# Performance work log

Measured on AMD Instinct MI355X. Metric: run time of the kernel, lower is better.

The kernel has to match this reference:

```python
import jax, jax.numpy as jnp
import numpy as np

B, T, U, V = 8, 128, 64, 1024
BLANK = V - 1  # blank=-1 resolves to last class index


def setup_inputs() -> dict:
    key = jax.random.key(0)
    k1, k2, k3, k4 = jax.random.split(key, 4)
    logits = jax.random.normal(k1, (B, T, U + 1, V), dtype=jnp.float32)
    targets = jax.random.randint(k2, (B, U), 0, V - 1, dtype=jnp.int32)  # exclude blank
    logit_lengths = jax.random.randint(k3, (B,), T // 2, T + 1, dtype=jnp.int32)
    target_lengths = jax.random.randint(k4, (B,), U // 2, U + 1, dtype=jnp.int32)
    return {
        "logits": logits,
        "targets": targets,
        "logit_lengths": logit_lengths,
        "target_lengths": target_lengths,
    }


def _rnnt_neglogp(logits, targets, logit_lengths, target_lengths, blank):
    """RNNT forward-variable DP (Graves 2012). Returns per-sample -log p(y|x)."""
    Bn, Tn, U1, Vn = logits.shape
    Un = U1 - 1
    lp = jax.nn.log_softmax(logits, axis=-1)  # fused_log_softmax=True
    lp_blank = lp[..., blank]                                  # (B, T, U+1)
    idx = jnp.broadcast_to(targets[:, None, :, None], (Bn, Tn, Un, 1))
    lp_emit = jnp.take_along_axis(lp[:, :, :Un, :], idx, axis=-1)[..., 0]  # (B, T, U)

    # alpha[t, u]: log-prob of emitting first u labels using first t frames.
    # alpha[0, u] = sum_{v<u} emit(0, v)
    row0 = jnp.concatenate(
        [jnp.zeros((Bn, 1), lp.dtype), jnp.cumsum(lp_emit[:, 0, :], axis=-1)], axis=1
    )  # (B, U+1)

    def inner(a_prev, x):
        # a[u] = logaddexp(alpha[t-1,u] + blank(t-1,u),  a[u-1] + emit(t,u-1))
        b_u, e_u = x
        a_new = jnp.logaddexp(b_u, a_prev + e_u)
        return a_new, a_new

    def outer(prev_row, x):
        blank_prev, emit_t = x  # (B, U+1), (B, U)
        b_term = prev_row + blank_prev  # vertical (blank) transition term
        _, rest = jax.lax.scan(
            inner, b_term[:, 0], (b_term[:, 1:].T, emit_t.T)
        )  # rest: (U, B)
        new_row = jnp.concatenate([b_term[:, :1], rest.T], axis=1)  # (B, U+1)
        return new_row, new_row

    xs = (
        jnp.swapaxes(lp_blank[:, :-1, :], 0, 1),  # (T-1, B, U+1)
        jnp.swapaxes(lp_emit[:, 1:, :], 0, 1),    # (T-1, B, U)
    )
    _, rows = jax.lax.scan(outer, row0, xs)
    alpha = jnp.concatenate([row0[None], rows], axis=0)  # (T, B, U+1)

    bidx = jnp.arange(Bn)
    t_last = logit_lengths - 1
    u_last = target_lengths
    a_end = alpha[t_last, bidx, u_last]
    final_blank = lp_blank[bidx, t_last, u_last]
    return -(a_end + final_blank)


def reference(logits, targets, logit_lengths, target_lengths):
    return _rnnt_neglogp(logits, targets, logit_lengths, target_lengths, BLANK)
```

## Files before the change

### kernel.cpp

```cpp
#include <hip/hip_runtime.h>
#include <hip/hip_bf16.h>

#define BB 8
#define TT 128
#define UU 64
#define VV 1024
#define U1 65
#define NROWS (BB * TT * U1)
#define NDIAG (TT + UU)
#define DSZ (NDIAG * U1)
#define CD 48
#define CH_F4 ((CD * U1) / 2)

__device__ __forceinline__ float wave_max64(float v) {
#pragma unroll
    for (int off = 32; off; off >>= 1) v = fmaxf(v, __shfl_xor(v, off, 64));
    return v;
}
__device__ __forceinline__ float wave_sum64(float v) {
#pragma unroll
    for (int off = 32; off; off >>= 1) v += __shfl_xor(v, off, 64);
    return v;
}

__global__ __launch_bounds__(256) void rnnt_lse_kernel(
    const float* __restrict__ logits, const int* __restrict__ targets,
    float2* __restrict__ P) {
    const int wave = threadIdx.x >> 6;
    const int lane = threadIdx.x & 63;
    const int row  = blockIdx.x * 4 + wave;
    const float4* p4 = (const float4*)(logits + (size_t)row * VV);

    float4 x0 = p4[lane];
    float4 x1 = p4[lane + 64];
    float4 x2 = p4[lane + 128];
    float4 x3 = p4[lane + 192];

    float m = fmaxf(fmaxf(fmaxf(x0.x, x0.y), fmaxf(x0.z, x0.w)),
                    fmaxf(fmaxf(x1.x, x1.y), fmaxf(x1.z, x1.w)));
    m = fmaxf(m, fmaxf(fmaxf(fmaxf(x2.x, x2.y), fmaxf(x2.z, x2.w)),
                       fmaxf(fmaxf(x3.x, x3.y), fmaxf(x3.z, x3.w))));
    m = wave_max64(m);

    float s = __expf(x0.x - m) + __expf(x0.y - m) + __expf(x0.z - m) + __expf(x0.w - m)
            + __expf(x1.x - m) + __expf(x1.y - m) + __expf(x1.z - m) + __expf(x1.w - m)
            + __expf(x2.x - m) + __expf(x2.y - m) + __expf(x2.z - m) + __expf(x2.w - m)
            + __expf(x3.x - m) + __expf(x3.y - m) + __expf(x3.z - m) + __expf(x3.w - m);
    s = wave_sum64(s);
    const float lse = m + __logf(s);

    const int b   = row / (TT * U1);
    const int rem = row - b * (TT * U1);
    const int t   = rem / U1;
    const int u   = rem - t * U1;

    const float blankv = __shfl(x3.w, 63, 64) - lse;
    float emitv = 0.f;
    if (u < UU) {
        const int tgt = targets[b * UU + u];
        const int q = tgt >> 2, grp = q >> 6, sl = q & 63, c = tgt & 3;
        float4 g4 = (grp == 0) ? x0 : (grp == 1) ? x1 : (grp == 2) ? x2 : x3;
        float cv = (c == 0) ? g4.x : (c == 1) ? g4.y : (c == 2) ? g4.z : g4.w;
        emitv = __shfl(cv, sl, 64) - lse;
    }
    if (lane == 0) P[(size_t)b * DSZ + (t + u) * U1 + u] = make_float2(blankv, emitv);
}

__global__ __launch_bounds__(64) void rnnt_dp_kernel(
    const float2* __restrict__ P, const int* __restrict__ logit_lengths,
    const int* __restrict__ target_lengths, float* __restrict__ out) {
    const int b = blockIdx.x;
    const int l = threadIdx.x;
    const float2* Pg = P + (size_t)b * DSZ;
    const int tl = logit_lengths[b] - 1;
    const int ul = target_lengths[b];

    __shared__ __align__(16) float2 sb[2][CD * U1];

    const float NEG = -1e30f;
    float aprev   = (l == 0) ? 0.f : NEG;
    float aprev64 = NEG;
    float res = 0.f;

    {
        const float4* g4 = (const float4*)Pg;
#pragma unroll
        for (int i = 0; i < 25; ++i) {
            int idx = i * 64 + l;
            if (idx < CH_F4) ((float4*)sb[0])[idx] = g4[idx];
        }
    }

    int d = 1;
    for (int g = 0; g < 4; ++g) {
        float4 v[25];
        if (g < 3) {
            const float4* g4 = (const float4*)Pg + (size_t)(g + 1) * CH_F4;
#pragma unroll
            for (int i = 0; i < 25; ++i) {
                int idx = i * 64 + l;
                if (idx < CH_F4) v[i] = g4[idx];
            }
        }
        const float2* buf = sb[g & 1];
#pragma unroll 1
        for (int i = 0; i < CD; ++i, ++d) {
            const int c = g * CD + i;
            if (c > NDIAG - 2) break;
            float2 pr  = buf[i * U1 + l];
            float2 p64 = buf[i * U1 + 64];
            float edl = __shfl_up(pr.y, 1, 64);
            float al  = __shfl_up(aprev, 1, 64);
            const int t = d - l;
            float va = (t >= 1) ? aprev + pr.x : NEG;
            float vb = (l >= 1) ? al + edl : NEG;
            float mm = fmaxf(va, vb);
            float r  = mm + __logf(__expf(va - mm) + __expf(vb - mm));
            r = (t >= 0 && t < TT) ? r : NEG;
            const int t64 = d - 64;
            float va64 = (t64 >= 1) ? aprev64 + p64.x : NEG;
            float vb64 = aprev + pr.y;
            float mm64 = fmaxf(va64, vb64);
            float r64  = mm64 + __logf(__expf(va64 - mm64) + __expf(vb64 - mm64));
            r64 = (t64 >= 0) ? r64 : NEG;
            if (d == tl + ul) {
                if (ul < 64) { if (l == ul) res = r; }
                else if (l == 63) res = r64;
            }
            aprev = r; aprev64 = r64;
        }
        if (g < 3) {
            float4* dst = (float4*)sb[(g + 1) & 1];
#pragma unroll
            for (int i = 0; i < 25; ++i) {
                int idx = i * 64 + l;
                if (idx < CH_F4) dst[idx] = v[i];
            }
        }
    }

    const float rr = __shfl(res, (ul < 64) ? ul : 63, 64);
    if (l == 0) out[b] = -(rr + Pg[(tl + ul) * U1 + ul].x);
}

extern "C" void kernel_launch(void* const* d_in, const int* in_sizes, int n_in,
                              void* d_out, int out_size, void* d_ws, size_t ws_size,
                              hipStream_t stream) {
    const float* logits         = (const float*)d_in[0];
    const int*   targets        = (const int*)d_in[1];
    const int*   logit_lengths  = (const int*)d_in[2];
    const int*   target_lengths = (const int*)d_in[3];
    float* outp = (float*)d_out;

    float2* P = (float2*)d_ws;

    rnnt_lse_kernel<<<NROWS / 4, 256, 0, stream>>>(logits, targets, P);
    rnnt_dp_kernel<<<BB, 64, 0, stream>>>(P, logit_lengths, target_lengths, outp);
}
```

Baseline: 433.7 us.

## Replace LDS chunk staging in DP kernel with register prefetch ring

The DP kernel no longer stages whole chunks of per-diagonal probabilities into double-buffered shared memory. Each lane now keeps a 16-deep register ring and issues the global load for diagonal c+16 while computing diagonal c, so load latency is hidden across the serial diagonal loop. The logaddexp is also rewritten as max + log(1+exp(min-max)), which needs one exponential instead of two on the dependency chain. The loop now runs one extra, harmless diagonal and uses more registers.

```diff
diff --git a/kernel.cpp b/kernel.cpp
--- a/kernel.cpp
+++ b/kernel.cpp
@@ -9,8 +9,6 @@
 #define NROWS (BB * TT * U1)
 #define NDIAG (TT + UU)
 #define DSZ (NDIAG * U1)
-#define CD 48
-#define CH_F4 ((CD * U1) / 2)
 
 __device__ __forceinline__ float wave_max64(float v) {
 #pragma unroll
@@ -66,76 +64,64 @@
     if (lane == 0) P[(size_t)b * DSZ + (t + u) * U1 + u] = make_float2(blankv, emitv);
 }
 
+#define PF 16
 __global__ __launch_bounds__(64) void rnnt_dp_kernel(
     const float2* __restrict__ P, const int* __restrict__ logit_lengths,
     const int* __restrict__ target_lengths, float* __restrict__ out) {
     const int b = blockIdx.x;
     const int l = threadIdx.x;
     const float2* Pg = P + (size_t)b * DSZ;
+    const float*  Pf = (const float*)Pg;
     const int tl = logit_lengths[b] - 1;
     const int ul = target_lengths[b];
-
-    __shared__ __align__(16) float2 sb[2][CD * U1];
 
     const float NEG = -1e30f;
     float aprev   = (l == 0) ? 0.f : NEG;
     float aprev64 = NEG;
     float res = 0.f;
 
-    {
-        const float4* g4 = (const float4*)Pg;
+    float2 prb[PF];
+    float  p64b[PF];
 #pragma unroll
-        for (int i = 0; i < 25; ++i) {
-            int idx = i * 64 + l;
-            if (idx < CH_F4) ((float4*)sb[0])[idx] = g4[idx];
-        }
+    for (int j = 0; j < PF; ++j) {
+        prb[j]  = Pg[j * U1 + l];
+        p64b[j] = Pf[(j * U1 + 64) * 2];
     }
 
     int d = 1;
-    for (int g = 0; g < 4; ++g) {
-        float4 v[25];
-        if (g < 3) {
-            const float4* g4 = (const float4*)Pg + (size_t)(g + 1) * CH_F4;
+#pragma unroll 1
+    for (int blk = 0; blk < NDIAG / PF; ++blk) {
 #pragma unroll
-            for (int i = 0; i < 25; ++i) {
-                int idx = i * 64 + l;
-                if (idx < CH_F4) v[i] = g4[idx];
+        for (int j = 0; j < PF; ++j, ++d) {
+            const int c = blk * PF + j;
+            const float2 pr  = prb[j];
+            const float pb64 = p64b[j];
+            const int cn = c + PF;
+            if (cn < NDIAG) {
+                prb[j]  = Pg[cn * U1 + l];
+                p64b[j] = Pf[(cn * U1 + 64) * 2];
             }
-        }
-        const float2* buf = sb[g & 1];
-#pragma unroll 1
-        for (int i = 0; i < CD; ++i, ++d) {
-            const int c = g * CD + i;
-            if (c > NDIAG - 2) break;
-            float2 pr  = buf[i * U1 + l];
-            float2 p64 = buf[i * U1 + 64];
             float edl = __shfl_up(pr.y, 1, 64);
             float al  = __shfl_up(aprev, 1, 64);
             const int t = d - l;
             float va = (t >= 1) ? aprev + pr.x : NEG;
             float vb = (l >= 1) ? al + edl : NEG;
             float mm = fmaxf(va, vb);
-            float r  = mm + __logf(__expf(va - mm) + __expf(vb - mm));
+            float lo = fminf(va, vb);
+            float r  = mm + __logf(1.f + __expf(lo - mm));
             r = (t >= 0 && t < TT) ? r : NEG;
             const int t64 = d - 64;
-            float va64 = (t64 >= 1) ? aprev64 + p64.x : NEG;
+            float va64 = (t64 >= 1) ? aprev64 + pb64 : NEG;
             float vb64 = aprev + pr.y;
             float mm64 = fmaxf(va64, vb64);
-            float r64  = mm64 + __logf(__expf(va64 - mm64) + __expf(vb64 - mm64));
+            float lo64 = fminf(va64, vb64);
+            float r64  = mm64 + __logf(1.f + __expf(lo64 - mm64));
             r64 = (t64 >= 0) ? r64 : NEG;
             if (d == tl + ul) {
                 if (ul < 64) { if (l == ul) res = r; }
                 else if (l == 63) res = r64;
             }
             aprev = r; aprev64 = r64;
-        }
-        if (g < 3) {
-            float4* dst = (float4*)sb[(g + 1) & 1];
-#pragma unroll
-            for (int i = 0; i < 25; ++i) {
-                int idx = i * 64 + l;
-                if (idx < CH_F4) dst[idx] = v[i];
-            }
         }
     }
 
```

New measurement: 430.3 us. About the same (-0.8%).
